# Kernel optimization log

Measured on AMD Instinct MI355X. Metric: run time of the kernel, lower is better.

## Reference

```python
import jax, jax.numpy as jnp
import numpy as np

B, S, D, H, DFF = 2, 4096, 512, 8, 2048
DK = D // H
EPS = 1e-6


def layer_norm(x, alpha, bias):
    # torch: (x - mean) / (std + eps), std unbiased (ddof=1), eps added to std
    mean = jnp.mean(x, axis=-1, keepdims=True)
    std = jnp.std(x, axis=-1, keepdims=True, ddof=1)
    return alpha * (x - mean) / (std + EPS) + bias


def setup_inputs() -> dict:
    key = jax.random.key(0)
    ks = jax.random.split(key, 10)
    s = 0.02
    return {
        "x": jax.random.normal(ks[0], (B, S, D), jnp.float32),
        "mask": jax.random.randint(ks[1], (S, S), 0, 2, jnp.int32),
        "w_q": jax.random.normal(ks[2], (D, D), jnp.float32) * s,
        "w_k": jax.random.normal(ks[3], (D, D), jnp.float32) * s,
        "w_v": jax.random.normal(ks[4], (D, D), jnp.float32) * s,
        "w_o": jax.random.normal(ks[5], (D, D), jnp.float32) * s,
        "w1": jax.random.normal(ks[6], (D, DFF), jnp.float32) * s,
        "b1": jnp.zeros((DFF,), jnp.float32),
        "w2": jax.random.normal(ks[7], (DFF, D), jnp.float32) * s,
        "b2": jnp.zeros((D,), jnp.float32),
        "ln1_a": jnp.ones((D,), jnp.float32),
        "ln1_b": jnp.zeros((D,), jnp.float32),
        "ln2_a": jnp.ones((D,), jnp.float32),
        "ln2_b": jnp.zeros((D,), jnp.float32),
    }


def reference(x, mask, w_q, w_k, w_v, w_o, w1, b1, w2, b2, ln1_a, ln1_b, ln2_a, ln2_b):
    # --- sublayer 0: pre-norm self-attention with residual (dropout=0/eval) ---
    h = layer_norm(x, ln1_a, ln1_b)                       # [B,S,D]
    q = (h @ w_q).reshape(B, S, H, DK)
    k = (h @ w_k).reshape(B, S, H, DK)
    v = (h @ w_v).reshape(B, S, H, DK)
    scores = jnp.einsum("bqhd,bkhd->bhqk", q, k) / jnp.sqrt(jnp.float32(DK))
    scores = jnp.where(mask[None, None, :, :] == 0, jnp.float32(-1e9), scores)
    attn = jax.nn.softmax(scores, axis=-1)                # [B,H,S,S]
    ctx = jnp.einsum("bhqk,bkhd->bqhd", attn, v).reshape(B, S, D)
    x = x + ctx @ w_o
    # --- sublayer 1: pre-norm FFN with residual ---
    h2 = layer_norm(x, ln2_a, ln2_b)
    ff = jax.nn.relu(h2 @ w1 + b1) @ w2 + b2
    return x + ff
```

## Files before the change

### kernel.cpp

```cpp
#include <hip/hip_runtime.h>
#include <hip/hip_bf16.h>
#include <stdint.h>

#define S_LEN 4096
#define DMODEL 512
#define NHEAD 8
#define DHEAD 64
#define NTOK 8192

typedef unsigned short ushort_t;
typedef __attribute__((ext_vector_type(8))) short short8;
typedef __attribute__((ext_vector_type(4))) float f32x4;
typedef unsigned long long u64;
typedef __attribute__((ext_vector_type(2))) unsigned uint2v;

__device__ __forceinline__ float bf2f(ushort_t h) {
    union { unsigned u; float f; } c; c.u = ((unsigned)h) << 16; return c.f;
}
__device__ __forceinline__ ushort_t f2bf(float f) {
    union { float f; unsigned u; } c; c.f = f;
    unsigned u = c.u + 0x7fffu + ((c.u >> 16) & 1u);
    return (ushort_t)(u >> 16);
}
__device__ __forceinline__ void glds16(const ushort_t* g, ushort_t* l) {
    __builtin_amdgcn_global_load_lds(
        (const __attribute__((address_space(1))) unsigned int*)g,
        (__attribute__((address_space(3))) unsigned int*)l, 16, 0, 0);
}

__global__ __launch_bounds__(256) void maskbits_kernel(const int* __restrict__ mask,
        u64* __restrict__ mb) {
    size_t id = (size_t)blockIdx.x * 256 + threadIdx.x;
    int v = mask[id];
    u64 bits = __ballot(v != 0);
    if ((threadIdx.x & 63) == 0) mb[id >> 6] = bits;
}

__global__ __launch_bounds__(256) void masktrans_kernel(const u64* __restrict__ mb,
        u64* __restrict__ mbT) {
    int wid = (int)(((size_t)blockIdx.x * 256 + threadIdx.x) >> 6);
    int lane = threadIdx.x & 63;
    int gq = wid >> 7, kt = wid & 127;
    int lr = lane & 15, lg = lane >> 4;
    int row = gq * 16 + lr;
    u64* outp = mbT + ((size_t)gq * 128 + kt) * 8;
#pragma unroll
    for (int t = 0; t < 2; t++)
#pragma unroll
        for (int r = 0; r < 4; r++) {
            int col = kt * 32 + t * 16 + lg * 4 + r;
            u64 w = mb[(size_t)row * 64 + (col >> 6)];
            u64 bb = __ballot((unsigned)((w >> (col & 63)) & 1));
            if (lane == t * 4 + r) outp[t * 4 + r] = bb;
        }
}

__global__ __launch_bounds__(256) void wtrans_all(const float* __restrict__ wq,
        const float* __restrict__ wk, const float* __restrict__ wv,
        const float* __restrict__ wo, const float* __restrict__ w1,
        const float* __restrict__ w2,
        ushort_t* wqT, ushort_t* wkT, ushort_t* wvT, ushort_t* woT,
        ushort_t* w1T, ushort_t* w2T) {
    __shared__ __attribute__((aligned(16))) ushort_t t[64][72];
    int z = blockIdx.z;
    const float* src; ushort_t* dst; int R, C;
    switch (z) {
        case 0: src = wq; dst = wqT; R = 512;  C = 512;  break;
        case 1: src = wk; dst = wkT; R = 512;  C = 512;  break;
        case 2: src = wv; dst = wvT; R = 512;  C = 512;  break;
        case 3: src = wo; dst = woT; R = 512;  C = 512;  break;
        case 4: src = w1; dst = w1T; R = 512;  C = 2048; break;
        default: src = w2; dst = w2T; R = 2048; C = 512; break;
    }
    int r0 = blockIdx.x * 64, c0 = blockIdx.y * 64;
    if (r0 >= R || c0 >= C) return;
    int tid = threadIdx.x;
    for (int i = tid; i < 4096; i += 256) {
        int r = i >> 6, c = i & 63;
        t[r][c] = f2bf(src[(size_t)(r0 + r) * C + c0 + c]);
    }
    __syncthreads();
    for (int i = tid; i < 512; i += 256) {
        int c = i >> 3, rb = i & 7;
        short8 vv;
#pragma unroll
        for (int j = 0; j < 8; j++) ((ushort_t*)&vv)[j] = t[rb * 8 + j][c];
        *(short8*)(dst + (size_t)(c0 + c) * R + r0 + rb * 8) = vv;
    }
}

__global__ __launch_bounds__(256) void ln_f32(const float* __restrict__ x,
        const float* __restrict__ ga, const float* __restrict__ be,
        ushort_t* __restrict__ out) {
    int tok = blockIdx.x * 4 + (threadIdx.x >> 6);
    int lane = threadIdx.x & 63;
    const float* xr = x + (size_t)tok * DMODEL + lane * 8;
    f32x4 v0 = *(const f32x4*)xr;
    f32x4 v1 = *(const f32x4*)(xr + 4);
    float f[8];
    float s = 0.f, s2 = 0.f;
#pragma unroll
    for (int i = 0; i < 8; i++) {
        f[i] = (i < 4) ? v0[i] : v1[i - 4];
        s += f[i]; s2 += f[i] * f[i];
    }
#pragma unroll
    for (int off = 1; off < 64; off <<= 1) {
        s += __shfl_xor(s, off);
        s2 += __shfl_xor(s2, off);
    }
    float mean = s * (1.f / DMODEL);
    float var = (s2 - (float)DMODEL * mean * mean) * (1.f / (DMODEL - 1));
    var = fmaxf(var, 0.f);
    float inv = 1.f / (sqrtf(var) + 1e-6f);
    short8 o;
#pragma unroll
    for (int i = 0; i < 8; i++) {
        float val = ga[lane * 8 + i] * (f[i] - mean) * inv + be[lane * 8 + i];
        ((ushort_t*)&o)[i] = f2bf(val);
    }
    *(short8*)(out + (size_t)tok * DMODEL + lane * 8) = o;
}

__global__ __launch_bounds__(256) void vtrans(const ushort_t* __restrict__ V,
        ushort_t* __restrict__ VT) {
    __shared__ __attribute__((aligned(16))) ushort_t t[64][72];
    int s0 = blockIdx.x * 64;
    int bh = blockIdx.y;
    int b = bh >> 3, h = bh & 7;
    int tid = threadIdx.x;
    const ushort_t* src = V + ((size_t)b * S_LEN + s0) * DMODEL + h * DHEAD;
    for (int i = tid; i < 512; i += 256) {
        int r = i >> 3, cb = i & 7;
        *(short8*)&t[r][cb * 8] = *(const short8*)(src + (size_t)r * DMODEL + cb * 8);
    }
    __syncthreads();
    ushort_t* dst = VT + (size_t)bh * DHEAD * S_LEN;
    for (int i = tid; i < 512; i += 256) {
        int d = i >> 3, rb = i & 7;
        short8 vv;
#pragma unroll
        for (int j = 0; j < 8; j++) ((ushort_t*)&vv)[j] = t[rb * 8 + j][d];
        *(short8*)(dst + (size_t)d * S_LEN + s0 + rb * 8) = vv;
    }
}

template <int MW, int NW>
__device__ __forceinline__ void gemm_body(const ushort_t* __restrict__ A,
        const ushort_t* __restrict__ BT, void* __restrict__ C,
        int N, int K, float scale, const float* __restrict__ bias,
        const float* __restrict__ res, int relu, int cf32,
        ushort_t* As, ushort_t* Bs, int m0, int n0, int aoff, int coff) {
    int tid = threadIdx.x;
    int wave = tid >> 6, lane = tid & 63;
    int wm = wave >> 1, wn = wave & 1;
    int lr = lane & 15, lg = lane >> 4;
    int srow = lane >> 3, spos = lane & 7;
    int kst = (spos ^ srow) * 8;
    int rdk = lr & 7;
    f32x4 acc[MW][NW];
#pragma unroll
    for (int i = 0; i < MW; i++)
#pragma unroll
        for (int j = 0; j < NW; j++) acc[i][j] = (f32x4){0.f, 0.f, 0.f, 0.f};

    const ushort_t* Ag = A + (size_t)(m0 - aoff) * K;
    const ushort_t* Bg = BT + (size_t)n0 * K;

    for (int k0 = 0; k0 < K; k0 += 64) {
        __syncthreads();
        for (int ia = wave; ia < 4 * MW; ia += 4)
            glds16(Ag + (size_t)(ia * 8 + srow) * K + k0 + kst, As + ia * 8 * 64);
        for (int ib = wave; ib < 4 * NW; ib += 4)
            glds16(Bg + (size_t)(ib * 8 + srow) * K + k0 + kst, Bs + ib * 8 * 64);
        __syncthreads();
        short8 af[MW][2], bfv[NW][2];
#pragma unroll
        for (int t = 0; t < MW; t++) {
            const ushort_t* ar = As + (size_t)(wm * 16 * MW + t * 16 + lr) * 64;
            af[t][0] = *(const short8*)(ar + ((lg ^ rdk) * 8));
            af[t][1] = *(const short8*)(ar + (((lg + 4) ^ rdk) * 8));
        }
#pragma unroll
        for (int t = 0; t < NW; t++) {
            const ushort_t* br = Bs + (size_t)(wn * 16 * NW + t * 16 + lr) * 64;
            bfv[t][0] = *(const short8*)(br + ((lg ^ rdk) * 8));
            bfv[t][1] = *(const short8*)(br + (((lg + 4) ^ rdk) * 8));
        }
#pragma unroll
        for (int i = 0; i < MW; i++)
#pragma unroll
            for (int j = 0; j < NW; j++) {
                acc[i][j] = __builtin_amdgcn_mfma_f32_16x16x32_bf16(af[i][0], bfv[j][0], acc[i][j], 0, 0, 0);
                acc[i][j] = __builtin_amdgcn_mfma_f32_16x16x32_bf16(af[i][1], bfv[j][1], acc[i][j], 0, 0, 0);
            }
    }
#pragma unroll
    for (int i = 0; i < MW; i++) {
        int row = m0 + wm * 16 * MW + i * 16 + lg * 4;
#pragma unroll
        for (int j = 0; j < NW; j++) {
            int col = n0 + wn * 16 * NW + j * 16 + lr;
            float bb = bias ? bias[col] : 0.f;
#pragma unroll
            for (int r = 0; r < 4; r++) {
                float v = acc[i][j][r] * scale + bb;
                if (relu) v = fmaxf(v, 0.f);
                if (res) v += res[(size_t)(row + r) * N + col];
                size_t cidx = (size_t)(row + r - coff) * N + col;
                if (cf32) ((float*)C)[cidx] = v;
                else      ((ushort_t*)C)[cidx] = f2bf(v);
            }
        }
    }
}

__global__ __launch_bounds__(256) void gemm_bt64(const ushort_t* __restrict__ A,
        const ushort_t* __restrict__ BT, void* __restrict__ C,
        int N, int K, float scale, const float* bias, const float* res, int relu,
        int cf32, int m_base, int aoff, int coff) {
    __shared__ __attribute__((aligned(16))) ushort_t As[64 * 64];
    __shared__ __attribute__((aligned(16))) ushort_t Bs[64 * 64];
    gemm_body<2, 2>(A, BT, C, N, K, scale, bias, res, relu, cf32, As, Bs,
                    m_base + blockIdx.x * 64, blockIdx.y * 64, aoff, coff);
}

__global__ __launch_bounds__(256) void gemm_qkv(const ushort_t* __restrict__ A,
        const ushort_t* __restrict__ wqT, const ushort_t* __restrict__ wkT,
        const ushort_t* __restrict__ wvT,
        ushort_t* __restrict__ Q, ushort_t* __restrict__ Kb, ushort_t* __restrict__ V) {
    __shared__ __attribute__((aligned(16))) ushort_t As[128 * 64];
    __shared__ __attribute__((aligned(16))) ushort_t Bs[128 * 64];
    int z = blockIdx.z;
    const ushort_t* W = (z == 0) ? wqT : ((z == 1) ? wkT : wvT);
    ushort_t* O = (z == 0) ? Q : ((z == 1) ? Kb : V);
    float sc = (z == 0) ? 0.18033688011112042f : 1.f;
    gemm_body<4, 4>(A, W, O, DMODEL, DMODEL, sc, nullptr, nullptr, 0, 0, As, Bs,
                    blockIdx.x * 128, blockIdx.y * 128, 0, 0);
}

__global__ __launch_bounds__(128, 4) void attn_kernel(const ushort_t* __restrict__ Q,
        const ushort_t* __restrict__ K, const ushort_t* __restrict__ VT,
        const u64* __restrict__ mbT, ushort_t* __restrict__ Opart,
        float* __restrict__ lpart) {
    __shared__ __attribute__((aligned(16))) ushort_t Ks[2][32 * 64];
    __shared__ __attribute__((aligned(16))) ushort_t Vs[2][64 * 32];
    int qt = blockIdx.x, h = blockIdx.y, zz = blockIdx.z;
    int b = zz >> 1, half = zz & 1;
    int tid = threadIdx.x;
    int wv = __builtin_amdgcn_readfirstlane(tid >> 6);
    int lane = tid & 63;
    int lr = lane & 15, lg = lane >> 4;
    size_t tokbase = (size_t)b * S_LEN;
    int q0 = qt * 64 + wv * 32;
    int k0 = half * (S_LEN / 2);

    const ushort_t* Qp = Q + (tokbase + q0) * DMODEL + h * DHEAD;
    short8 qf[2][2];
#pragma unroll
    for (int u = 0; u < 2; u++) {
        qf[u][0] = *(const short8*)(Qp + (size_t)(u * 16 + lr) * DMODEL + lg * 8);
        qf[u][1] = *(const short8*)(Qp + (size_t)(u * 16 + lr) * DMODEL + 32 + lg * 8);
    }
    f32x4 o[2][4];
#pragma unroll
    for (int u = 0; u < 2; u++)
#pragma unroll
        for (int td = 0; td < 4; td++) o[u][td] = (f32x4){0.f, 0.f, 0.f, 0.f};
    f32x4 den[2] = {(f32x4){0.f, 0.f, 0.f, 0.f}, (f32x4){0.f, 0.f, 0.f, 0.f}};
    short8 ones8;
#pragma unroll
    for (int j = 0; j < 8; j++) ((ushort_t*)&ones8)[j] = 0x3F80;

    int srow = lane >> 3, spos = lane & 7;
    int srow2 = lane >> 2, spos2 = lane & 3;
    int kst = (spos ^ srow) * 8;
    int vst = (spos2 ^ ((srow2 >> 1) & 3)) * 8;
    int rdk = lr & 7;
    int rdv = (lr >> 1) & 3;

    const ushort_t* kgl = K + (tokbase + k0) * DMODEL + h * DHEAD
                          + (size_t)srow * DMODEL + kst;
    const ushort_t* vgl = VT + (size_t)(b * NHEAD + h) * DHEAD * S_LEN
                          + (size_t)srow2 * S_LEN + k0 + vst;
    const u64* mq0 = mbT + (((size_t)(q0 >> 4)) * 128 + half * 64) * 8;
    const u64* mq1 = mq0 + 128 * 8;

    if (wv == 0) {
        glds16(kgl + (size_t)0 * DMODEL, &Ks[0][0 * 64]);
        glds16(kgl + (size_t)8 * DMODEL, &Ks[0][8 * 64]);
        glds16(vgl + (size_t)0 * S_LEN, &Vs[0][0 * 32]);
        glds16(vgl + (size_t)16 * S_LEN, &Vs[0][16 * 32]);
    } else {
        glds16(kgl + (size_t)16 * DMODEL, &Ks[0][16 * 64]);
        glds16(kgl + (size_t)24 * DMODEL, &Ks[0][24 * 64]);
        glds16(vgl + (size_t)32 * S_LEN, &Vs[0][32 * 32]);
        glds16(vgl + (size_t)48 * S_LEN, &Vs[0][48 * 32]);
    }

    const int NIT = (S_LEN / 2) / 32;
#pragma unroll 1
    for (int kt = 0; kt < NIT; kt++) {
        int cur = kt & 1;
        const u64* m0 = mq0 + (size_t)kt * 8;
        const u64* m1 = mq1 + (size_t)kt * 8;
        __builtin_amdgcn_s_barrier();
        if (kt + 1 < NIT) {
            const ushort_t* kgn = kgl + (size_t)(kt + 1) * 32 * DMODEL;
            const ushort_t* vgn = vgl + (kt + 1) * 32;
            if (wv == 0) {
                glds16(kgn + (size_t)0 * DMODEL, &Ks[cur ^ 1][0 * 64]);
                glds16(kgn + (size_t)8 * DMODEL, &Ks[cur ^ 1][8 * 64]);
                glds16(vgn + (size_t)0 * S_LEN, &Vs[cur ^ 1][0 * 32]);
                glds16(vgn + (size_t)16 * S_LEN, &Vs[cur ^ 1][16 * 32]);
            } else {
                glds16(kgn + (size_t)16 * DMODEL, &Ks[cur ^ 1][16 * 64]);
                glds16(kgn + (size_t)24 * DMODEL, &Ks[cur ^ 1][24 * 64]);
                glds16(vgn + (size_t)32 * S_LEN, &Vs[cur ^ 1][32 * 32]);
                glds16(vgn + (size_t)48 * S_LEN, &Vs[cur ^ 1][48 * 32]);
            }
            __builtin_amdgcn_s_waitcnt(3956);
        } else {
            __builtin_amdgcn_s_waitcnt(3952);
        }
        __builtin_amdgcn_s_barrier();
        __builtin_amdgcn_s_setprio(1);
        const ushort_t* Kb_ = Ks[cur];
        const ushort_t* Vb_ = Vs[cur];
        f32x4 s[2][2];
#pragma unroll
        for (int t = 0; t < 2; t++) {
            const ushort_t* kr = Kb_ + (t * 16 + lr) * 64;
            short8 kf0 = *(const short8*)(kr + ((lg ^ rdk) * 8));
            short8 kf1 = *(const short8*)(kr + (((lg + 4) ^ rdk) * 8));
#pragma unroll
            for (int u = 0; u < 2; u++) {
                f32x4 z = (f32x4){0.f, 0.f, 0.f, 0.f};
                z = __builtin_amdgcn_mfma_f32_16x16x32_bf16(kf0, qf[u][0], z, 0, 0, 0);
                z = __builtin_amdgcn_mfma_f32_16x16x32_bf16(kf1, qf[u][1], z, 0, 0, 0);
                s[t][u] = z;
            }
        }
#pragma unroll
        for (int u = 0; u < 2; u++) {
            const u64* mu = u ? m1 : m0;
#pragma unroll
            for (int r = 0; r < 4; r++) {
                float p0, p1;
                asm("v_exp_f32 %0, %1\n\ts_nop 0" : "=v"(p0) : "v"(s[0][u][r]));
                asm("v_exp_f32 %0, %1\n\ts_nop 0" : "=v"(p1) : "v"(s[1][u][r]));
                asm("v_cndmask_b32 %0, 0, %1, %2" : "=v"(p0) : "v"(p0), "s"(mu[r]));
                asm("v_cndmask_b32 %0, 0, %1, %2" : "=v"(p1) : "v"(p1), "s"(mu[4 + r]));
                s[0][u][r] = p0; s[1][u][r] = p1;
            }
        }
        short8 vf[4];
#pragma unroll
        for (int td = 0; td < 4; td++)
            vf[td] = *(const short8*)(Vb_ + (td * 16 + lr) * 32 + ((lg ^ rdv) * 8));
#pragma unroll
        for (int u = 0; u < 2; u++) {
            unsigned c00, c01, c10, c11;
            asm("v_cvt_pk_bf16_f32 %0, %1, %2" : "=v"(c00) : "v"(s[0][u][0]), "v"(s[0][u][1]));
            asm("v_cvt_pk_bf16_f32 %0, %1, %2" : "=v"(c01) : "v"(s[0][u][2]), "v"(s[0][u][3]));
            asm("v_cvt_pk_bf16_f32 %0, %1, %2" : "=v"(c10) : "v"(s[1][u][0]), "v"(s[1][u][1]));
            asm("v_cvt_pk_bf16_f32 %0, %1, %2" : "=v"(c11) : "v"(s[1][u][2]), "v"(s[1][u][3]));
            auto r0 = __builtin_amdgcn_permlane32_swap(c00, c10, false, false);
            auto r1 = __builtin_amdgcn_permlane32_swap(c01, c11, false, false);
            auto p0 = __builtin_amdgcn_permlane16_swap(r0[0], r0[1], false, false);
            auto p1 = __builtin_amdgcn_permlane16_swap(r1[0], r1[1], false, false);
            union { unsigned u32[4]; short8 s8; } pk;
            pk.u32[0] = p0[0]; pk.u32[1] = p1[0]; pk.u32[2] = p0[1]; pk.u32[3] = p1[1];
            short8 pf = pk.s8;
#pragma unroll
            for (int td = 0; td < 4; td++)
                o[u][td] = __builtin_amdgcn_mfma_f32_16x16x32_bf16(pf, vf[td], o[u][td], 0, 0, 0);
            den[u] = __builtin_amdgcn_mfma_f32_16x16x32_bf16(pf, ones8, den[u], 0, 0, 0);
        }
        __builtin_amdgcn_s_setprio(0);
    }
    float* lp = lpart + (size_t)half * (NHEAD * 2 * S_LEN)
                + (size_t)(b * NHEAD + h) * S_LEN + q0;
    if (lr == 0) {
#pragma unroll
        for (int u = 0; u < 2; u++)
#pragma unroll
            for (int r = 0; r < 4; r++)
                lp[u * 16 + lg * 4 + r] = den[u][r];
    }
    ushort_t* Op = Opart + (size_t)half * NTOK * DMODEL;
#pragma unroll
    for (int u = 0; u < 2; u++) {
        size_t rowb = (tokbase + q0 + u * 16 + lg * 4) * DMODEL + h * DHEAD;
#pragma unroll
        for (int td = 0; td < 4; td++) {
            int cc = td * 16 + lr;
            Op[rowb + 0 * DMODEL + cc] = f2bf(o[u][td][0]);
            Op[rowb + 1 * DMODEL + cc] = f2bf(o[u][td][1]);
            Op[rowb + 2 * DMODEL + cc] = f2bf(o[u][td][2]);
            Op[rowb + 3 * DMODEL + cc] = f2bf(o[u][td][3]);
        }
    }
}

__global__ __launch_bounds__(256) void attn_combine(const ushort_t* __restrict__ Oa,
        const ushort_t* __restrict__ Ob, const float* __restrict__ la,
        const float* __restrict__ lb, ushort_t* __restrict__ ctx) {
    size_t idx = ((size_t)blockIdx.x * 256 + threadIdx.x) * 8;
    size_t tok = idx >> 9;
    int col = (int)(idx & 511);
    int h = col >> 6;
    int b = (int)(tok >> 12);
    int q = (int)(tok & 4095);
    size_t li = (size_t)(b * NHEAD + h) * S_LEN + q;
    float inv = 1.f / (la[li] + lb[li]);
    short8 va = *(const short8*)(Oa + idx);
    short8 vb = *(const short8*)(Ob + idx);
    short8 oo;
#pragma unroll
    for (int j = 0; j < 8; j++)
        ((ushort_t*)&oo)[j] = f2bf((bf2f(((const ushort_t*)&va)[j])
                                  + bf2f(((const ushort_t*)&vb)[j])) * inv);
    *(short8*)(ctx + idx) = oo;
}

extern "C" void kernel_launch(void* const* d_in, const int* in_sizes, int n_in,
                              void* d_out, int out_size, void* d_ws, size_t ws_size,
                              hipStream_t stream) {
    (void)in_sizes; (void)n_in; (void)out_size; (void)ws_size;
    const float* x    = (const float*)d_in[0];
    const int*   mask = (const int*)d_in[1];
    const float* w_q  = (const float*)d_in[2];
    const float* w_k  = (const float*)d_in[3];
    const float* w_v  = (const float*)d_in[4];
    const float* w_o  = (const float*)d_in[5];
    const float* w1   = (const float*)d_in[6];
    const float* b1   = (const float*)d_in[7];
    const float* w2   = (const float*)d_in[8];
    const float* b2   = (const float*)d_in[9];
    const float* l1a  = (const float*)d_in[10];
    const float* l1b  = (const float*)d_in[11];
    const float* l2a  = (const float*)d_in[12];
    const float* l2b  = (const float*)d_in[13];

    char* ws = (char*)d_ws;
    const size_t MB = 1024 * 1024;
    const size_t KB = 1024;
    ushort_t* w1T  = (ushort_t*)(ws + 0);
    ushort_t* w2T  = (ushort_t*)(ws + 2 * MB);
    ushort_t* wqT  = (ushort_t*)(ws + 4 * MB);
    ushort_t* wkT  = (ushort_t*)(ws + 4 * MB + 512 * KB);
    ushort_t* wvT  = (ushort_t*)(ws + 5 * MB);
    ushort_t* woT  = (ushort_t*)(ws + 5 * MB + 512 * KB);
    ushort_t* ff1  = (ushort_t*)(ws + 6 * MB);
    ushort_t* h    = (ushort_t*)(ws + 22 * MB);
    ushort_t* VTb  = h;
    ushort_t* h2   = h;
    ushort_t* Qb   = (ushort_t*)(ws + 30 * MB);
    float*    x2f  = (float*)(ws + 30 * MB);
    ushort_t* Kb   = (ushort_t*)(ws + 38 * MB);
    ushort_t* Vb   = (ushort_t*)(ws + 46 * MB);
    ushort_t* ctx  = Vb;
    ushort_t* Opart = ff1;
    float*    lpart = (float*)wqT;
    u64*      mb   = (u64*)d_out;
    u64*      mbT  = (u64*)((char*)d_out + 2 * MB);
    float*    out  = (float*)d_out;

    dim3 blk(256);
    maskbits_kernel<<<dim3(65536), blk, 0, stream>>>(mask, mb);
    masktrans_kernel<<<dim3(8192), blk, 0, stream>>>(mb, mbT);
    wtrans_all<<<dim3(32, 32, 6), blk, 0, stream>>>(w_q, w_k, w_v, w_o, w1, w2,
            wqT, wkT, wvT, woT, w1T, w2T);
    ln_f32<<<dim3(NTOK / 4), blk, 0, stream>>>(x, l1a, l1b, h);
    gemm_qkv<<<dim3(64, 4, 3), blk, 0, stream>>>(h, wqT, wkT, wvT, Qb, Kb, Vb);
    vtrans<<<dim3(64, 16), blk, 0, stream>>>(Vb, VTb);
    attn_kernel<<<dim3(64, 8, 4), dim3(128), 0, stream>>>(Qb, Kb, VTb,
            mbT, Opart, lpart);
    attn_combine<<<dim3(2048), blk, 0, stream>>>(Opart,
            Opart + (size_t)NTOK * DMODEL, lpart, lpart + NHEAD * 2 * S_LEN, ctx);
    gemm_bt64<<<dim3(128, 8), blk, 0, stream>>>(ctx, woT, x2f, 512, 512, 1.f,
            nullptr, x, 0, 1, 0, 0, 0);
    ln_f32<<<dim3(NTOK / 4), blk, 0, stream>>>(x2f, l2a, l2b, h2);
    gemm_bt64<<<dim3(64, 32), blk, 0, stream>>>(h2, w1T, ff1, 2048, 512, 1.f,
            b1, nullptr, 1, 0, 0, 0, 0);
    gemm_bt64<<<dim3(64, 8), blk, 0, stream>>>(ff1, w2T, out, 512, 2048, 1.f,
            b2, x2f, 0, 1, 0, 0, 0);
    gemm_bt64<<<dim3(64, 32), blk, 0, stream>>>(h2, w1T, ff1, 2048, 512, 1.f,
            b1, nullptr, 1, 0, 4096, 0, 4096);
    gemm_bt64<<<dim3(64, 8), blk, 0, stream>>>(ff1, w2T, out, 512, 2048, 1.f,
            b2, x2f, 0, 1, 4096, 4096, 0);
}
```

Baseline: 410.8 us.

## Split attention key range into four partitions instead of two

The attention kernel now splits the key sequence into four quarters instead of two halves, doubling the grid to 4096 blocks so more workgroups are in flight. Each block writes its partial output and denominators to one of four buffers, and the combine kernel sums all four. Workspace and output buffers are rearranged to hold the extra partials. The setprio calls around the MFMA section are removed. In exchange the combine pass moves more partial-output traffic, each block pays the Q-fragment load and prologue over a shorter loop, and the partial sums round through bf16 twice as often.

```diff
diff --git a/kernel.cpp b/kernel.cpp
--- a/kernel.cpp
+++ b/kernel.cpp
@@ -241,19 +241,20 @@
 
 __global__ __launch_bounds__(128, 4) void attn_kernel(const ushort_t* __restrict__ Q,
         const ushort_t* __restrict__ K, const ushort_t* __restrict__ VT,
-        const u64* __restrict__ mbT, ushort_t* __restrict__ Opart,
-        float* __restrict__ lpart) {
+        const u64* __restrict__ mbT, ushort_t* __restrict__ O0,
+        ushort_t* __restrict__ O1, ushort_t* __restrict__ O2,
+        ushort_t* __restrict__ O3, float* __restrict__ lpart) {
     __shared__ __attribute__((aligned(16))) ushort_t Ks[2][32 * 64];
     __shared__ __attribute__((aligned(16))) ushort_t Vs[2][64 * 32];
     int qt = blockIdx.x, h = blockIdx.y, zz = blockIdx.z;
-    int b = zz >> 1, half = zz & 1;
+    int b = zz >> 2, qr = zz & 3;
     int tid = threadIdx.x;
     int wv = __builtin_amdgcn_readfirstlane(tid >> 6);
     int lane = tid & 63;
     int lr = lane & 15, lg = lane >> 4;
     size_t tokbase = (size_t)b * S_LEN;
     int q0 = qt * 64 + wv * 32;
-    int k0 = half * (S_LEN / 2);
+    int k0 = qr * (S_LEN / 4);
 
     const ushort_t* Qp = Q + (tokbase + q0) * DMODEL + h * DHEAD;
     short8 qf[2][2];
@@ -283,7 +284,7 @@
                           + (size_t)srow * DMODEL + kst;
     const ushort_t* vgl = VT + (size_t)(b * NHEAD + h) * DHEAD * S_LEN
                           + (size_t)srow2 * S_LEN + k0 + vst;
-    const u64* mq0 = mbT + (((size_t)(q0 >> 4)) * 128 + half * 64) * 8;
+    const u64* mq0 = mbT + (((size_t)(q0 >> 4)) * 128 + qr * 32) * 8;
     const u64* mq1 = mq0 + 128 * 8;
 
     if (wv == 0) {
@@ -298,7 +299,7 @@
         glds16(vgl + (size_t)48 * S_LEN, &Vs[0][48 * 32]);
     }
 
-    const int NIT = (S_LEN / 2) / 32;
+    const int NIT = (S_LEN / 4) / 32;
 #pragma unroll 1
     for (int kt = 0; kt < NIT; kt++) {
         int cur = kt & 1;
@@ -324,7 +325,6 @@
             __builtin_amdgcn_s_waitcnt(3952);
         }
         __builtin_amdgcn_s_barrier();
-        __builtin_amdgcn_s_setprio(1);
         const ushort_t* Kb_ = Ks[cur];
         const ushort_t* Vb_ = Vs[cur];
         f32x4 s[2][2];
@@ -377,9 +377,8 @@
                 o[u][td] = __builtin_amdgcn_mfma_f32_16x16x32_bf16(pf, vf[td], o[u][td], 0, 0, 0);
             den[u] = __builtin_amdgcn_mfma_f32_16x16x32_bf16(pf, ones8, den[u], 0, 0, 0);
         }
-        __builtin_amdgcn_s_setprio(0);
-    }
-    float* lp = lpart + (size_t)half * (NHEAD * 2 * S_LEN)
+    }
+    float* lp = lpart + (size_t)qr * (NHEAD * 2 * S_LEN)
                 + (size_t)(b * NHEAD + h) * S_LEN + q0;
     if (lr == 0) {
 #pragma unroll
@@ -388,7 +387,7 @@
             for (int r = 0; r < 4; r++)
                 lp[u * 16 + lg * 4 + r] = den[u][r];
     }
-    ushort_t* Op = Opart + (size_t)half * NTOK * DMODEL;
+    ushort_t* Op = (qr == 0) ? O0 : ((qr == 1) ? O1 : ((qr == 2) ? O2 : O3));
 #pragma unroll
     for (int u = 0; u < 2; u++) {
         size_t rowb = (tokbase + q0 + u * 16 + lg * 4) * DMODEL + h * DHEAD;
@@ -404,8 +403,10 @@
 }
 
 __global__ __launch_bounds__(256) void attn_combine(const ushort_t* __restrict__ Oa,
-        const ushort_t* __restrict__ Ob, const float* __restrict__ la,
-        const float* __restrict__ lb, ushort_t* __restrict__ ctx) {
+        const ushort_t* __restrict__ Ob, const ushort_t* __restrict__ Oc,
+        const ushort_t* __restrict__ Od, const float* __restrict__ la,
+        const float* __restrict__ lb, const float* __restrict__ lc,
+        const float* __restrict__ ld, ushort_t* __restrict__ ctx) {
     size_t idx = ((size_t)blockIdx.x * 256 + threadIdx.x) * 8;
     size_t tok = idx >> 9;
     int col = (int)(idx & 511);
@@ -413,14 +414,18 @@
     int b = (int)(tok >> 12);
     int q = (int)(tok & 4095);
     size_t li = (size_t)(b * NHEAD + h) * S_LEN + q;
-    float inv = 1.f / (la[li] + lb[li]);
+    float inv = 1.f / (la[li] + lb[li] + lc[li] + ld[li]);
     short8 va = *(const short8*)(Oa + idx);
     short8 vb = *(const short8*)(Ob + idx);
+    short8 vc = *(const short8*)(Oc + idx);
+    short8 vd = *(const short8*)(Od + idx);
     short8 oo;
 #pragma unroll
     for (int j = 0; j < 8; j++)
         ((ushort_t*)&oo)[j] = f2bf((bf2f(((const ushort_t*)&va)[j])
-                                  + bf2f(((const ushort_t*)&vb)[j])) * inv);
+                                  + bf2f(((const ushort_t*)&vb)[j])
+                                  + bf2f(((const ushort_t*)&vc)[j])
+                                  + bf2f(((const ushort_t*)&vd)[j])) * inv);
     *(short8*)(ctx + idx) = oo;
 }
 
@@ -452,6 +457,11 @@
     ushort_t* wkT  = (ushort_t*)(ws + 4 * MB + 512 * KB);
     ushort_t* wvT  = (ushort_t*)(ws + 5 * MB);
     ushort_t* woT  = (ushort_t*)(ws + 5 * MB + 512 * KB);
+    float*    lpart = (float*)(ws + 4 * MB);
+    ushort_t* O0   = (ushort_t*)(ws + 6 * MB);
+    ushort_t* O1   = (ushort_t*)(ws + 14 * MB);
+    ushort_t* O3   = (ushort_t*)(ws + 46 * MB);
+    ushort_t* ctx  = O0;
     ushort_t* ff1  = (ushort_t*)(ws + 6 * MB);
     ushort_t* h    = (ushort_t*)(ws + 22 * MB);
     ushort_t* VTb  = h;
@@ -460,11 +470,9 @@
     float*    x2f  = (float*)(ws + 30 * MB);
     ushort_t* Kb   = (ushort_t*)(ws + 38 * MB);
     ushort_t* Vb   = (ushort_t*)(ws + 46 * MB);
-    ushort_t* ctx  = Vb;
-    ushort_t* Opart = ff1;
-    float*    lpart = (float*)wqT;
-    u64*      mb   = (u64*)d_out;
-    u64*      mbT  = (u64*)((char*)d_out + 2 * MB);
+    ushort_t* O2   = (ushort_t*)d_out;
+    u64*      mbT  = (u64*)((char*)d_out + 8 * MB);
+    u64*      mb   = (u64*)((char*)d_out + 10 * MB);
     float*    out  = (float*)d_out;
 
     dim3 blk(256);
@@ -475,10 +483,10 @@
     ln_f32<<<dim3(NTOK / 4), blk, 0, stream>>>(x, l1a, l1b, h);
     gemm_qkv<<<dim3(64, 4, 3), blk, 0, stream>>>(h, wqT, wkT, wvT, Qb, Kb, Vb);
     vtrans<<<dim3(64, 16), blk, 0, stream>>>(Vb, VTb);
-    attn_kernel<<<dim3(64, 8, 4), dim3(128), 0, stream>>>(Qb, Kb, VTb,
-            mbT, Opart, lpart);
-    attn_combine<<<dim3(2048), blk, 0, stream>>>(Opart,
-            Opart + (size_t)NTOK * DMODEL, lpart, lpart + NHEAD * 2 * S_LEN, ctx);
+    attn_kernel<<<dim3(64, 8, 8), dim3(128), 0, stream>>>(Qb, Kb, VTb,
+            mbT, O0, O1, O2, O3, lpart);
+    attn_combine<<<dim3(2048), blk, 0, stream>>>(O0, O1, O2, O3,
+            lpart, lpart + 65536, lpart + 2 * 65536, lpart + 3 * 65536, ctx);
     gemm_bt64<<<dim3(128, 8), blk, 0, stream>>>(ctx, woT, x2f, 512, 512, 1.f,
             nullptr, x, 0, 1, 0, 0, 0);
     ln_f32<<<dim3(NTOK / 4), blk, 0, stream>>>(x2f, l2a, l2b, h2);
```

After: 423.1 us. +3.0%, slower.

## Split-K the FFN down-projection with atomic adds and drop attention setprio

Applied to the files above, without the earlier changes.

The W2 GEMM (K=2048) is split into two K halves across blockIdx.z, and each half accumulates into the output with float atomicAdd. The output is pre-initialised with the residual plus bias by a new elementwise kernel. This doubles the block count of a GEMM that previously launched only 512 blocks, improving occupancy, at the cost of an extra kernel, atomic traffic and a nondeterministic summation order. Separately, the s_setprio raise/lower around the attention compute loop is removed.

```diff
diff --git a/kernel.cpp b/kernel.cpp
--- a/kernel.cpp
+++ b/kernel.cpp
@@ -122,6 +122,15 @@
     *(short8*)(out + (size_t)tok * DMODEL + lane * 8) = o;
 }
 
+__global__ __launch_bounds__(256) void out_init(const float* __restrict__ x2f,
+        const float* __restrict__ b2, float* __restrict__ out) {
+    size_t i = ((size_t)blockIdx.x * 256 + threadIdx.x) * 4;
+    f32x4 v = *(const f32x4*)(x2f + i);
+    f32x4 bb = *(const f32x4*)(b2 + (int)(i & 511));
+    v = v + bb;
+    *(f32x4*)(out + i) = v;
+}
+
 __global__ __launch_bounds__(256) void vtrans(const ushort_t* __restrict__ V,
         ushort_t* __restrict__ VT) {
     __shared__ __attribute__((aligned(16))) ushort_t t[64][72];
@@ -148,8 +157,9 @@
 template <int MW, int NW>
 __device__ __forceinline__ void gemm_body(const ushort_t* __restrict__ A,
         const ushort_t* __restrict__ BT, void* __restrict__ C,
-        int N, int K, float scale, const float* __restrict__ bias,
-        const float* __restrict__ res, int relu, int cf32,
+        int N, int Klen, int kstride, int kbeg, float scale,
+        const float* __restrict__ bias, const float* __restrict__ res,
+        int relu, int cf32, int atomicc,
         ushort_t* As, ushort_t* Bs, int m0, int n0, int aoff, int coff) {
     int tid = threadIdx.x;
     int wave = tid >> 6, lane = tid & 63;
@@ -164,15 +174,15 @@
 #pragma unroll
         for (int j = 0; j < NW; j++) acc[i][j] = (f32x4){0.f, 0.f, 0.f, 0.f};
 
-    const ushort_t* Ag = A + (size_t)(m0 - aoff) * K;
-    const ushort_t* Bg = BT + (size_t)n0 * K;
-
-    for (int k0 = 0; k0 < K; k0 += 64) {
+    const ushort_t* Ag = A + (size_t)(m0 - aoff) * kstride + kbeg;
+    const ushort_t* Bg = BT + (size_t)n0 * kstride + kbeg;
+
+    for (int k0 = 0; k0 < Klen; k0 += 64) {
         __syncthreads();
         for (int ia = wave; ia < 4 * MW; ia += 4)
-            glds16(Ag + (size_t)(ia * 8 + srow) * K + k0 + kst, As + ia * 8 * 64);
+            glds16(Ag + (size_t)(ia * 8 + srow) * kstride + k0 + kst, As + ia * 8 * 64);
         for (int ib = wave; ib < 4 * NW; ib += 4)
-            glds16(Bg + (size_t)(ib * 8 + srow) * K + k0 + kst, Bs + ib * 8 * 64);
+            glds16(Bg + (size_t)(ib * 8 + srow) * kstride + k0 + kst, Bs + ib * 8 * 64);
         __syncthreads();
         short8 af[MW][2], bfv[NW][2];
 #pragma unroll
@@ -208,8 +218,9 @@
                 if (relu) v = fmaxf(v, 0.f);
                 if (res) v += res[(size_t)(row + r) * N + col];
                 size_t cidx = (size_t)(row + r - coff) * N + col;
-                if (cf32) ((float*)C)[cidx] = v;
-                else      ((ushort_t*)C)[cidx] = f2bf(v);
+                if (atomicc)   atomicAdd((float*)C + cidx, v);
+                else if (cf32) ((float*)C)[cidx] = v;
+                else           ((ushort_t*)C)[cidx] = f2bf(v);
             }
         }
     }
@@ -221,8 +232,18 @@
         int cf32, int m_base, int aoff, int coff) {
     __shared__ __attribute__((aligned(16))) ushort_t As[64 * 64];
     __shared__ __attribute__((aligned(16))) ushort_t Bs[64 * 64];
-    gemm_body<2, 2>(A, BT, C, N, K, scale, bias, res, relu, cf32, As, Bs,
+    gemm_body<2, 2>(A, BT, C, N, K, K, 0, scale, bias, res, relu, cf32, 0, As, Bs,
                     m_base + blockIdx.x * 64, blockIdx.y * 64, aoff, coff);
+}
+
+__global__ __launch_bounds__(256) void gemm_w2sk(const ushort_t* __restrict__ A,
+        const ushort_t* __restrict__ BT, float* __restrict__ C,
+        int m_base, int aoff) {
+    __shared__ __attribute__((aligned(16))) ushort_t As[64 * 64];
+    __shared__ __attribute__((aligned(16))) ushort_t Bs[64 * 64];
+    int kbeg = blockIdx.z * 1024;
+    gemm_body<2, 2>(A, BT, C, 512, 1024, 2048, kbeg, 1.f, nullptr, nullptr, 0, 1, 1,
+                    As, Bs, m_base + blockIdx.x * 64, blockIdx.y * 64, aoff, 0);
 }
 
 __global__ __launch_bounds__(256) void gemm_qkv(const ushort_t* __restrict__ A,
@@ -235,8 +256,8 @@
     const ushort_t* W = (z == 0) ? wqT : ((z == 1) ? wkT : wvT);
     ushort_t* O = (z == 0) ? Q : ((z == 1) ? Kb : V);
     float sc = (z == 0) ? 0.18033688011112042f : 1.f;
-    gemm_body<4, 4>(A, W, O, DMODEL, DMODEL, sc, nullptr, nullptr, 0, 0, As, Bs,
-                    blockIdx.x * 128, blockIdx.y * 128, 0, 0);
+    gemm_body<4, 4>(A, W, O, DMODEL, DMODEL, DMODEL, 0, sc, nullptr, nullptr, 0, 0, 0,
+                    As, Bs, blockIdx.x * 128, blockIdx.y * 128, 0, 0);
 }
 
 __global__ __launch_bounds__(128, 4) void attn_kernel(const ushort_t* __restrict__ Q,
@@ -324,7 +345,6 @@
             __builtin_amdgcn_s_waitcnt(3952);
         }
         __builtin_amdgcn_s_barrier();
-        __builtin_amdgcn_s_setprio(1);
         const ushort_t* Kb_ = Ks[cur];
         const ushort_t* Vb_ = Vs[cur];
         f32x4 s[2][2];
@@ -377,7 +397,6 @@
                 o[u][td] = __builtin_amdgcn_mfma_f32_16x16x32_bf16(pf, vf[td], o[u][td], 0, 0, 0);
             den[u] = __builtin_amdgcn_mfma_f32_16x16x32_bf16(pf, ones8, den[u], 0, 0, 0);
         }
-        __builtin_amdgcn_s_setprio(0);
     }
     float* lp = lpart + (size_t)half * (NHEAD * 2 * S_LEN)
                 + (size_t)(b * NHEAD + h) * S_LEN + q0;
@@ -482,12 +501,11 @@
     gemm_bt64<<<dim3(128, 8), blk, 0, stream>>>(ctx, woT, x2f, 512, 512, 1.f,
             nullptr, x, 0, 1, 0, 0, 0);
     ln_f32<<<dim3(NTOK / 4), blk, 0, stream>>>(x2f, l2a, l2b, h2);
+    out_init<<<dim3(4096), blk, 0, stream>>>(x2f, b2, out);
     gemm_bt64<<<dim3(64, 32), blk, 0, stream>>>(h2, w1T, ff1, 2048, 512, 1.f,
             b1, nullptr, 1, 0, 0, 0, 0);
-    gemm_bt64<<<dim3(64, 8), blk, 0, stream>>>(ff1, w2T, out, 512, 2048, 1.f,
-            b2, x2f, 0, 1, 0, 0, 0);
+    gemm_w2sk<<<dim3(64, 8, 2), blk, 0, stream>>>(ff1, w2T, out, 0, 0);
     gemm_bt64<<<dim3(64, 32), blk, 0, stream>>>(h2, w1T, ff1, 2048, 512, 1.f,
             b1, nullptr, 1, 0, 4096, 0, 4096);
-    gemm_bt64<<<dim3(64, 8), blk, 0, stream>>>(ff1, w2T, out, 512, 2048, 1.f,
-            b2, x2f, 0, 1, 4096, 4096, 0);
-}
+    gemm_w2sk<<<dim3(64, 8, 2), blk, 0, stream>>>(ff1, w2T, out, 4096, 4096);
+}
```

After: 405.8 us. No clear change (-1.2%).
